# Performance work log

Measured on AMD Instinct MI355X. Metric: run time of the kernel, lower is better.

Reference implementation:

```python
import jax, jax.numpy as jnp
import numpy as np

B, T, N, C = 32, 12, 1024, 2   # batch, lookback window, n_series, in_channels
D, H, K, OUT = 16, 64, 2, 12   # embedding_dim, rnn_units, cheb_k, out_dim (horizon)


def setup_inputs() -> dict:
    key = jax.random.key(0)
    ks = jax.random.split(key, 12)
    p = lambda k, sh, s=0.1: jax.random.normal(k, sh, dtype=jnp.float32) * s
    return {
        "source": jax.random.normal(ks[0], (B, T, N, C), dtype=jnp.float32),
        "node_emb": p(ks[1], (N, D), 0.3),
        # layer 0: dim_in = C + H
        "gate_w0": p(ks[2], (D, K, C + H, 2 * H)),
        "gate_b0": p(ks[3], (D, 2 * H)),
        "upd_w0": p(ks[4], (D, K, C + H, H)),
        "upd_b0": p(ks[5], (D, H)),
        # layer 1: dim_in = H + H
        "gate_w1": p(ks[6], (D, K, 2 * H, 2 * H)),
        "gate_b1": p(ks[7], (D, 2 * H)),
        "upd_w1": p(ks[8], (D, K, 2 * H, H)),
        "upd_b1": p(ks[9], (D, H)),
        # end_conv: Conv2d(1, OUT*out_channels, kernel=(1,H)) == linear over hidden dim
        "conv_w": p(ks[10], (OUT, H)),
        "conv_b": p(ks[11], (OUT,)),
    }


def _supports(node_emb):
    # softmax(relu(E E^T)) row-normalized adaptive adjacency; Chebyshev stack (K, N, N)
    A = jax.nn.softmax(jax.nn.relu(node_emb @ node_emb.T), axis=1)
    s = [jnp.eye(N, dtype=A.dtype), A]
    for _ in range(2, K):
        s.append(2.0 * A @ s[-1] - s[-2])
    return jnp.stack(s, axis=0)


def _gcn(x, node_emb, w_pool, b_pool, supports):
    # x: (B, N, Cin); per-node adaptive weights from pools
    w = jnp.einsum('nd,dkio->nkio', node_emb, w_pool)     # (N, K, Cin, Cout)
    b = node_emb @ b_pool                                 # (N, Cout)
    xg = jnp.einsum('knm,bmc->bnkc', supports, x)         # (B, N, K, Cin)
    return jnp.einsum('bnki,nkio->bno', xg, w) + b


def _layer(x_seq, node_emb, supports, gw, gb, uw, ub):
    # x_seq: (B, T, N, Cin) -> (B, T, N, H) via GRU-style AGCRN cell, scanned over T
    def step(state, x_t):
        inp = jnp.concatenate([x_t, state], axis=-1)
        zr = jax.nn.sigmoid(_gcn(inp, node_emb, gw, gb, supports))
        z, r = jnp.split(zr, 2, axis=-1)
        cand = jnp.concatenate([x_t, z * state], axis=-1)
        hc = jnp.tanh(_gcn(cand, node_emb, uw, ub, supports))
        h = r * state + (1.0 - r) * hc
        return h, h

    init = jnp.zeros((x_seq.shape[0], N, H), dtype=x_seq.dtype)
    _, hs = jax.lax.scan(step, init, jnp.swapaxes(x_seq, 0, 1))
    return jnp.swapaxes(hs, 0, 1)


def reference(source, node_emb, gate_w0, gate_b0, upd_w0, upd_b0,
              gate_w1, gate_b1, upd_w1, upd_b1, conv_w, conv_b,
              teacher_forcing_ratio=0):
    sup = _supports(node_emb)  # adaptive supports depend only on static node_emb
    h1 = _layer(source, node_emb, sup, gate_w0, gate_b0, upd_w0, upd_b0)
    h2 = _layer(h1, node_emb, sup, gate_w1, gate_b1, upd_w1, upd_b1)
    last = h2[:, -1]  # (B, N, H)
    # end_conv over hidden dim -> (B, OUT, N); out_channels==1 so squeeze folds away
    out = jnp.einsum('bnh,oh->bon', last, conv_w) + conv_b[None, :, None]
    return out
```

## Files before the change

### kernel.cpp

```cpp
#include <hip/hip_runtime.h>
#include <hip/hip_fp16.h>


typedef _Float16 f16x8 __attribute__((ext_vector_type(8)));
typedef _Float16 f16x4 __attribute__((ext_vector_type(4)));
typedef float f32x4 __attribute__((ext_vector_type(4)));

__global__ __launch_bounds__(256) void compute_A_kernel(const float* __restrict__ E,
                                                        __half* __restrict__ Ah) {
  int n = blockIdx.x;
  int tid = threadIdx.x;
  __shared__ float red[256];
  float en[16];
#pragma unroll
  for (int d = 0; d < 16; ++d) en[d] = E[n * 16 + d];
  float v[4];
#pragma unroll
  for (int q = 0; q < 4; ++q) {
    int m = tid + q * 256;
    const float* Em = E + m * 16;
    float dot = 0.f;
#pragma unroll
    for (int d = 0; d < 16; ++d) dot += en[d] * Em[d];
    v[q] = fmaxf(dot, 0.f);
  }
  float mx = fmaxf(fmaxf(v[0], v[1]), fmaxf(v[2], v[3]));
  red[tid] = mx; __syncthreads();
  for (int s = 128; s > 0; s >>= 1) { if (tid < s) red[tid] = fmaxf(red[tid], red[tid + s]); __syncthreads(); }
  mx = red[0];
  __syncthreads();
  float e[4], sum = 0.f;
#pragma unroll
  for (int q = 0; q < 4; ++q) { e[q] = expf(v[q] - mx); sum += e[q]; }
  red[tid] = sum; __syncthreads();
  for (int s = 128; s > 0; s >>= 1) { if (tid < s) red[tid] += red[tid + s]; __syncthreads(); }
  float inv = 1.f / red[0];
#pragma unroll
  for (int q = 0; q < 4; ++q) Ah[(size_t)n * 1024 + tid + q * 256] = __float2half(e[q] * inv);
}

__global__ __launch_bounds__(256) void pool_t16_kernel(const float* __restrict__ gw0,
                                                       const float* __restrict__ uw0,
                                                       const float* __restrict__ gw1,
                                                       const float* __restrict__ uw1,
                                                       __half* __restrict__ poolT16) {
  int rg = blockIdx.x;
  const float* pool; int F, Fp, O; size_t jbase; int kk, jj;
  if (rg < 160)      { pool = gw0; F = 66;  Fp = 80;  O = 128; jbase = 0;     kk = rg / 80;          jj = rg % 80; }
  else if (rg < 320) { pool = uw0; F = 66;  Fp = 80;  O = 64;  jbase = 20480; kk = (rg - 160) / 80;  jj = (rg - 160) % 80; }
  else if (rg < 576) { pool = gw1; F = 128; Fp = 128; O = 128; jbase = 30720; kk = (rg - 320) / 128; jj = (rg - 320) % 128; }
  else               { pool = uw1; F = 128; Fp = 128; O = 64;  jbase = 63488; kk = (rg - 576) / 128; jj = (rg - 576) % 128; }
  int o = threadIdx.x;
  if (o >= O) return;
  int i;
  if (F == Fp) i = jj;
  else i = (jj < 64) ? jj + 2 : (jj < 66 ? jj - 64 : -1);
  f16x8 a = {}, b = {}, zz = {};
  if (i >= 0) {
#pragma unroll
    for (int d = 0; d < 8; ++d)
      a[d] = (_Float16)pool[(((size_t)d * 2 + kk) * F + i) * O + o];
#pragma unroll
    for (int d = 8; d < 16; ++d)
      b[d - 8] = (_Float16)pool[(((size_t)d * 2 + kk) * F + i) * O + o];
  }
  size_t j = jbase + (size_t)o * (2 * Fp) + (size_t)kk * Fp + jj;
  _Float16* outp = (_Float16*)poolT16 + j * 32;
  *(f16x8*)outp = a;
  *(f16x8*)(outp + 8) = b;
  *(f16x8*)(outp + 16) = zz;
  *(f16x8*)(outp + 24) = zz;
}

__global__ __launch_bounds__(256) void prelude_misc_kernel(
    const float* __restrict__ E, __half* __restrict__ E16,
    const float* __restrict__ gb0, const float* __restrict__ ub0,
    const float* __restrict__ gb1, const float* __restrict__ ub1,
    float* __restrict__ Bg0, float* __restrict__ Bu0,
    float* __restrict__ Bg1, float* __restrict__ Bu1,
    const float* __restrict__ src, __half* __restrict__ x16,
    float4* __restrict__ zero_p) {
  int bid = blockIdx.x;
  if (bid < 8192) {
    int i = bid * 256 + threadIdx.x;
    zero_p[i] = float4{0.f, 0.f, 0.f, 0.f};
    return;
  }
  bid -= 8192;
  if (bid < 384) {
    int t0 = bid >> 5, b = bid & 31;
    const float* s = src + (size_t)(b * 12 + t0) * 2048;
    __half* dst = x16 + t0 * 64 + b * 2;
    for (int nn = threadIdx.x; nn < 1024; nn += 256) {
      float2 v = *(const float2*)(s + nn * 2);
      *(__half2*)(dst + (size_t)nn * 768) = __floats2half2_rn(v.x, v.y);
    }
    return;
  }
  bid -= 384;
  if (bid < 1536) {
    int tid = bid * 256 + threadIdx.x;
    if (tid >= 1024 * 384) return;
    int n = tid / 384, c = tid - n * 384;
    const float* pool; float* outp; int O, o;
    if (c < 128)      { pool = gb0; outp = Bg0; O = 128; o = c; }
    else if (c < 192) { pool = ub0; outp = Bu0; O = 64;  o = c - 128; }
    else if (c < 320) { pool = gb1; outp = Bg1; O = 128; o = c - 192; }
    else              { pool = ub1; outp = Bu1; O = 64;  o = c - 320; }
    const float* En = E + n * 16;
    float a = 0.f;
#pragma unroll
    for (int d = 0; d < 16; ++d) a += En[d] * pool[d * O + o];
    outp[n * O + o] = a;
    return;
  }
  bid -= 1536;
  {
    int t = bid * 256 + threadIdx.x;
    if (t >= 1024 * 32) return;
    int d = t & 31;
    E16[t] = (d < 16) ? __float2half(E[(t >> 5) * 16 + d]) : __half(0);
  }
}

__global__ __launch_bounds__(256) void make_wt_mfma_kernel(
    const __half* __restrict__ E16g, const __half* __restrict__ poolT16g,
    __half* __restrict__ WtG0, __half* __restrict__ WtU0,
    __half* __restrict__ WtG1, __half* __restrict__ WtU1) {
  __shared__ __align__(16) _Float16 Es[64][40];
  __shared__ __align__(16) _Float16 wbuf[64][264];
  const _Float16* E16 = (const _Float16*)E16g;
  const _Float16* pT = (const _Float16*)poolT16g;
  int bx = blockIdx.x;
  __half* Wt; int OK, jbase;
  if (bx < 80)       { Wt = WtG0; OK = 128 * 160; jbase = bx * 256; }
  else if (bx < 120) { Wt = WtU0; OK = 64 * 160;  jbase = (bx - 80) * 256; }
  else if (bx < 248) { Wt = WtG1; OK = 128 * 256; jbase = (bx - 120) * 256; }
  else               { Wt = WtU1; OK = 64 * 256;  jbase = (bx - 248) * 256; }
  int jglob0 = bx * 256;
  int n0 = blockIdx.y * 64;
  {
    int r = threadIdx.x >> 2, ch = (threadIdx.x & 3) * 8;
    *(f16x8*)&Es[r][ch] = *(const f16x8*)(E16 + (size_t)(n0 + r) * 32 + ch);
  }
  __syncthreads();
  int wave = threadIdx.x >> 6, lane = threadIdx.x & 63;
  int fm = lane & 15, fg = lane >> 4;
  f16x8 af[4];
#pragma unroll
  for (int i = 0; i < 4; ++i) af[i] = *(const f16x8*)&Es[i * 16 + fm][fg * 8];
  f32x4 acc[4][4] = {};
#pragma unroll
  for (int j = 0; j < 4; ++j) {
    int jc = jglob0 + wave * 64 + j * 16 + fm;
    f16x8 bf = *(const f16x8*)(pT + (size_t)jc * 32 + fg * 8);
#pragma unroll
    for (int i = 0; i < 4; ++i)
      acc[i][j] = __builtin_amdgcn_mfma_f32_16x16x32_f16(af[i], bf, acc[i][j], 0, 0, 0);
  }
#pragma unroll
  for (int i = 0; i < 4; ++i)
#pragma unroll
    for (int j = 0; j < 4; ++j)
#pragma unroll
      for (int r = 0; r < 4; ++r)
        wbuf[i * 16 + fg * 4 + r][wave * 64 + j * 16 + fm] = (_Float16)acc[i][j][r];
  __syncthreads();
  for (int idx = threadIdx.x; idx < 64 * 32; idx += 256) {
    int nsub = idx >> 5, pos = (idx & 31) * 8;
    *(float4*)(Wt + (size_t)(n0 + nsub) * OK + jbase + pos) = *(float4*)&wbuf[nsub][pos];
  }
}

__global__ __launch_bounds__(256) void gemm_nt_kernel(
    const __half* __restrict__ Ahg, const __half* __restrict__ X0g,
    const __half* __restrict__ X1g, __half* __restrict__ Yg,
    int Nc, int cstride, int split) {
  __shared__ __align__(16) _Float16 As[64][136];
  __shared__ __align__(16) _Float16 Bs[64][144];
  const _Float16* __restrict__ Ah = (const _Float16*)Ahg;
  _Float16* __restrict__ Y = (_Float16*)Yg;
  int tid = threadIdx.x;
  int row0 = blockIdx.y * 64;
  int col0 = blockIdx.x * 64;
  const _Float16* __restrict__ Xsrc =
      (col0 < split) ? (const _Float16*)X0g : (const _Float16*)X1g;
  int colg = (col0 < split) ? col0 : col0 - split;
  int wave = tid >> 6, lane = tid & 63;
  int wm = wave & 1, wn = wave >> 1;
  int fm = lane & 15, fg = lane >> 4;

  int sr = tid >> 2, sc = (tid & 3) * 32;
  const _Float16* pa = Ah + (size_t)(row0 + sr) * 1024 + sc;
  int kq = tid & 31, cg = tid >> 5;
  int kb = 4 * kq;
  const _Float16* pb = Xsrc + (size_t)kb * cstride + colg + cg * 8;
  int chunk = kq >> 1;
  int kin = (kq & 1) * 4;

  f16x8 ra[4], rb[4];
#pragma unroll
  for (int c = 0; c < 4; ++c) ra[c] = *(const f16x8*)(pa + c * 8);
#pragma unroll
  for (int r = 0; r < 4; ++r) rb[r] = *(const f16x8*)(pb + (size_t)r * cstride);

  f32x4 acc[2][2] = {};
  for (int k0 = 0; k0 < 1024; k0 += 128) {
#pragma unroll
    for (int c = 0; c < 4; ++c) *(f16x8*)&As[sr][sc + c * 8] = ra[c];
#pragma unroll
    for (int i = 0; i < 8; ++i) {
      int c = cg * 8 + i;
      f16x4 p;
      p[0] = rb[0][i]; p[1] = rb[1][i]; p[2] = rb[2][i]; p[3] = rb[3][i];
      *(f16x4*)&Bs[c][((chunk ^ (c & 7)) << 3) + kin] = p;
    }
    __syncthreads();
    if (k0 + 128 < 1024) {
#pragma unroll
      for (int c = 0; c < 4; ++c) ra[c] = *(const f16x8*)(pa + k0 + 128 + c * 8);
#pragma unroll
      for (int r = 0; r < 4; ++r)
        rb[r] = *(const f16x8*)(pb + (size_t)(k0 + 128 + r) * cstride);
    }
#pragma unroll
    for (int kc = 0; kc < 4; ++kc) {
      int ck = kc * 4 + fg;
      f16x8 af[2], bf[2];
#pragma unroll
      for (int i = 0; i < 2; ++i)
        af[i] = *(const f16x8*)&As[wm * 32 + i * 16 + fm][kc * 32 + fg * 8];
#pragma unroll
      for (int j = 0; j < 2; ++j) {
        int cl = wn * 32 + j * 16 + fm;
        bf[j] = *(const f16x8*)&Bs[cl][(ck ^ (cl & 7)) << 3];
      }
#pragma unroll
      for (int i = 0; i < 2; ++i)
#pragma unroll
        for (int j = 0; j < 2; ++j)
          acc[i][j] = __builtin_amdgcn_mfma_f32_16x16x32_f16(af[i], bf[j], acc[i][j], 0, 0, 0);
    }
    __syncthreads();
  }
#pragma unroll
  for (int i = 0; i < 2; ++i) {
#pragma unroll
    for (int j = 0; j < 2; ++j) {
      int col = col0 + wn * 32 + j * 16 + fm;
      int rbase = row0 + wm * 32 + i * 16 + fg * 4;
#pragma unroll
      for (int r = 0; r < 4; ++r)
        Y[(size_t)(rbase + r) * Nc + col] = (_Float16)acc[i][j][r];
    }
  }
}

__global__ __launch_bounds__(256) void gemm_nt128_kernel(
    const __half* __restrict__ Ahg, const __half* __restrict__ X0g,
    const __half* __restrict__ X1g, __half* __restrict__ Yg,
    int Nc, int cstride, int split) {
  __shared__ __align__(16) _Float16 As[64][136];
  __shared__ __align__(16) _Float16 Bs[128][144];
  const _Float16* __restrict__ Ah = (const _Float16*)Ahg;
  _Float16* __restrict__ Y = (_Float16*)Yg;
  int tid = threadIdx.x;
  int row0 = blockIdx.y * 64;
  int col0 = blockIdx.x * 128;
  const _Float16* __restrict__ Xsrc =
      (col0 < split) ? (const _Float16*)X0g : (const _Float16*)X1g;
  int colg = (col0 < split) ? col0 : col0 - split;
  int wave = tid >> 6, lane = tid & 63;
  int fm = lane & 15, fg = lane >> 4;

  int sr = tid >> 2, sc = (tid & 3) * 32;
  const _Float16* pa = Ah + (size_t)(row0 + sr) * 1024 + sc;
  int kq = tid & 31, cg = tid >> 5;
  int kb = 4 * kq;
  const _Float16* pb = Xsrc + (size_t)kb * cstride + colg + cg * 16;
  int chunk = kq >> 1;
  int kin = (kq & 1) * 4;

  f16x8 ra[4], rb[4][2];
#pragma unroll
  for (int c = 0; c < 4; ++c) ra[c] = *(const f16x8*)(pa + c * 8);
#pragma unroll
  for (int r = 0; r < 4; ++r)
#pragma unroll
    for (int h = 0; h < 2; ++h)
      rb[r][h] = *(const f16x8*)(pb + (size_t)r * cstride + h * 8);

  f32x4 acc[4][2] = {};
  for (int k0 = 0; k0 < 1024; k0 += 128) {
#pragma unroll
    for (int c = 0; c < 4; ++c) *(f16x8*)&As[sr][sc + c * 8] = ra[c];
#pragma unroll
    for (int h = 0; h < 2; ++h)
#pragma unroll
      for (int i = 0; i < 8; ++i) {
        int c = cg * 16 + h * 8 + i;
        f16x4 p;
        p[0] = rb[0][h][i]; p[1] = rb[1][h][i]; p[2] = rb[2][h][i]; p[3] = rb[3][h][i];
        *(f16x4*)&Bs[c][((chunk ^ (c & 7)) << 3) + kin] = p;
      }
    __syncthreads();
    if (k0 + 128 < 1024) {
#pragma unroll
      for (int c = 0; c < 4; ++c) ra[c] = *(const f16x8*)(pa + k0 + 128 + c * 8);
#pragma unroll
      for (int r = 0; r < 4; ++r)
#pragma unroll
        for (int h = 0; h < 2; ++h)
          rb[r][h] = *(const f16x8*)(pb + (size_t)(k0 + 128 + r) * cstride + h * 8);
    }
#pragma unroll
    for (int kc = 0; kc < 4; ++kc) {
      int ck = kc * 4 + fg;
      f16x8 af[4], bf[2];
#pragma unroll
      for (int i = 0; i < 4; ++i)
        af[i] = *(const f16x8*)&As[i * 16 + fm][kc * 32 + fg * 8];
#pragma unroll
      for (int j = 0; j < 2; ++j) {
        int cl = wave * 32 + j * 16 + fm;
        bf[j] = *(const f16x8*)&Bs[cl][(ck ^ (cl & 7)) << 3];
      }
#pragma unroll
      for (int i = 0; i < 4; ++i)
#pragma unroll
        for (int j = 0; j < 2; ++j)
          acc[i][j] = __builtin_amdgcn_mfma_f32_16x16x32_f16(af[i], bf[j], acc[i][j], 0, 0, 0);
    }
    __syncthreads();
  }
#pragma unroll
  for (int i = 0; i < 4; ++i) {
#pragma unroll
    for (int j = 0; j < 2; ++j) {
      int col = col0 + wave * 32 + j * 16 + fm;
      int rbase = row0 + i * 16 + fg * 4;
#pragma unroll
      for (int r = 0; r < 4; ++r)
        Y[(size_t)(rbase + r) * Nc + col] = (_Float16)acc[i][j][r];
    }
  }
}

__device__ __forceinline__ f16x8 ld_g0(const __half* __restrict__ h16,
                                       const __half* __restrict__ YBD, int n, int idx) {
  int b = idx >> 4, part = (idx >> 3) & 1, ch = idx & 7;
  const _Float16* s = part ? (const _Float16*)YBD + (size_t)n * 4096 + b * 64 + ch * 8
                           : (const _Float16*)h16 + (size_t)n * 2048 + b * 64 + ch * 8;
  return *(const f16x8*)s;
}
__device__ __forceinline__ f16x8 ld_u0(const __half* __restrict__ zh0,
                                       const __half* __restrict__ YCE, int n, int idx) {
  int b = idx >> 4, part = (idx >> 3) & 1, ch = idx & 7;
  const _Float16* s = part ? (const _Float16*)YCE + (size_t)n * 4096 + 2048 + b * 64 + ch * 8
                           : (const _Float16*)zh0 + (size_t)n * 2048 + b * 64 + ch * 8;
  return *(const f16x8*)s;
}

__device__ __forceinline__ void gate0_body(
    _Float16* Xs, int n, int t,
    f16x8 pre0, f16x8 pre1, float2 xv, unsigned axu,
    const __half* __restrict__ Wtg, const float* __restrict__ Bg,
    const float* __restrict__ h32, __half* __restrict__ zh0, __half* __restrict__ r0) {
  constexpr int KIP = 160, STRIDE = 168;
  {
    int b0 = t >> 4, p0 = (t >> 3) & 1, c0 = t & 7;
    *(f16x8*)&Xs[b0 * STRIDE + p0 * 80 + c0 * 8] = pre0;
    int idx = t + 256;
    int b1 = idx >> 4, p1 = (idx >> 3) & 1, c1 = idx & 7;
    *(f16x8*)&Xs[b1 * STRIDE + p1 * 80 + c1 * 8] = pre1;
  }
  if (t < 32) {
    Xs[t * STRIDE + 64] = (_Float16)xv.x;
    Xs[t * STRIDE + 65] = (_Float16)xv.y;
    *(unsigned*)&Xs[t * STRIDE + 144] = axu;
  }
  for (int idx = t; idx < 896; idx += 256) {
    int b = idx / 28, jj = idx % 28;
    int col = (jj < 14) ? 66 + jj : 132 + jj;
    Xs[b * STRIDE + col] = (_Float16)0.f;
  }
  __syncthreads();
  int wave = t >> 6, lane = t & 63;
  int fm = lane & 15, fg = lane >> 4;
  f32x4 acc[2][2] = {};
  const _Float16* Wn = (const _Float16*)Wtg + ((size_t)n * 128 + wave * 32) * KIP;
  __builtin_amdgcn_s_setprio(1);
#pragma unroll
  for (int kc = 0; kc < KIP / 32; ++kc) {
    f16x8 af[2], bf[2];
#pragma unroll
    for (int i = 0; i < 2; ++i)
      af[i] = *(const f16x8*)&Xs[(i * 16 + fm) * STRIDE + kc * 32 + fg * 8];
#pragma unroll
    for (int j = 0; j < 2; ++j)
      bf[j] = *(const f16x8*)(Wn + (size_t)(j * 16 + fm) * KIP + kc * 32 + fg * 8);
#pragma unroll
    for (int i = 0; i < 2; ++i)
#pragma unroll
      for (int j = 0; j < 2; ++j)
        acc[i][j] = __builtin_amdgcn_mfma_f32_16x16x32_f16(af[i], bf[j], acc[i][j], 0, 0, 0);
  }
  __builtin_amdgcn_s_setprio(0);
  const float* Bn = Bg + n * 128;
#pragma unroll
  for (int j = 0; j < 2; ++j) {
    int o = wave * 32 + j * 16 + fm;
    float bias = Bn[o];
#pragma unroll
    for (int i = 0; i < 2; ++i)
#pragma unroll
      for (int r = 0; r < 4; ++r) {
        int b = i * 16 + fg * 4 + r;
        float s = 1.f / (1.f + __expf(-(acc[i][j][r] + bias)));
        size_t base = (size_t)n * 2048 + b * 64;
        if (o < 64) zh0[base + o] = __float2half(s * h32[base + o]);
        else        r0[base + o - 64] = __float2half(s);
      }
  }
}

__device__ __forceinline__ void upd0_body(
    _Float16* Xs, int n, int t,
    f16x8 pre0, f16x8 pre1, float2 xv, unsigned axu,
    const __half* __restrict__ Wtg, const float* __restrict__ Bu,
    const __half* __restrict__ r0, float* __restrict__ h32, __half* __restrict__ h16) {
  constexpr int KIP = 160, STRIDE = 168;
  {
    int b0 = t >> 4, p0 = (t >> 3) & 1, c0 = t & 7;
    *(f16x8*)&Xs[b0 * STRIDE + p0 * 80 + c0 * 8] = pre0;
    int idx = t + 256;
    int b1 = idx >> 4, p1 = (idx >> 3) & 1, c1 = idx & 7;
    *(f16x8*)&Xs[b1 * STRIDE + p1 * 80 + c1 * 8] = pre1;
  }
  if (t < 32) {
    Xs[t * STRIDE + 64] = (_Float16)xv.x;
    Xs[t * STRIDE + 65] = (_Float16)xv.y;
    *(unsigned*)&Xs[t * STRIDE + 144] = axu;
  }
  for (int idx = t; idx < 896; idx += 256) {
    int b = idx / 28, jj = idx % 28;
    int col = (jj < 14) ? 66 + jj : 132 + jj;
    Xs[b * STRIDE + col] = (_Float16)0.f;
  }
  __syncthreads();
  int wave = t >> 6, lane = t & 63;
  int fm = lane & 15, fg = lane >> 4;
  f32x4 acc[2] = {};
  const _Float16* Wn = (const _Float16*)Wtg + ((size_t)n * 64 + wave * 16) * KIP;
  __builtin_amdgcn_s_setprio(1);
#pragma unroll
  for (int kc = 0; kc < KIP / 32; ++kc) {
    f16x8 bf = *(const f16x8*)(Wn + (size_t)fm * KIP + kc * 32 + fg * 8);
#pragma unroll
    for (int i = 0; i < 2; ++i) {
      f16x8 af = *(const f16x8*)&Xs[(i * 16 + fm) * STRIDE + kc * 32 + fg * 8];
      acc[i] = __builtin_amdgcn_mfma_f32_16x16x32_f16(af, bf, acc[i], 0, 0, 0);
    }
  }
  __builtin_amdgcn_s_setprio(0);
  int o = wave * 16 + fm;
  float bias = Bu[n * 64 + o];
#pragma unroll
  for (int i = 0; i < 2; ++i)
#pragma unroll
    for (int r = 0; r < 4; ++r) {
      int b = i * 16 + fg * 4 + r;
      float x = acc[i][r] + bias;
      x = fminf(fmaxf(x, -15.f), 15.f);
      float e = __expf(2.f * x);
      float hc = (e - 1.f) / (e + 1.f);
      size_t base = (size_t)n * 2048 + b * 64;
      float rr = __half2float(r0[base + o]);
      float hnew = rr * h32[base + o] + (1.f - rr) * hc;
      h32[base + o] = hnew;
      h16[base + o] = __float2half(hnew);
    }
}

__global__ __launch_bounds__(256) void gate0_kernel(
    const __half* __restrict__ h16, const __half* __restrict__ YBD,
    const float* __restrict__ src, const __half* __restrict__ Axt, int tstep,
    const __half* __restrict__ Wtg, const float* __restrict__ Bg,
    const float* __restrict__ h32, __half* __restrict__ zh0, __half* __restrict__ r0) {
  __shared__ __align__(16) _Float16 Xs[32 * 168];
  int n = blockIdx.x, t = threadIdx.x;
  f16x8 p0 = ld_g0(h16, YBD, n, t);
  f16x8 p1 = ld_g0(h16, YBD, n, t + 256);
  float2 xv = {}; unsigned ax = 0;
  if (t < 32) {
    xv = *(const float2*)(src + ((size_t)(t * 12 + tstep) * 1024 + n) * 2);
    ax = *(const unsigned*)((const _Float16*)Axt + (size_t)n * 768 + tstep * 64 + t * 2);
  }
  gate0_body(Xs, n, t, p0, p1, xv, ax, Wtg, Bg, h32, zh0, r0);
}

__global__ __launch_bounds__(256) void upd0_kernel(
    const __half* __restrict__ zh0, const __half* __restrict__ YCE,
    const float* __restrict__ src, const __half* __restrict__ Axt, int tstep,
    const __half* __restrict__ Wtg, const float* __restrict__ Bu,
    const __half* __restrict__ r0, float* __restrict__ h32, __half* __restrict__ h16) {
  __shared__ __align__(16) _Float16 Xs[32 * 168];
  int n = blockIdx.x, t = threadIdx.x;
  f16x8 p0 = ld_u0(zh0, YCE, n, t);
  f16x8 p1 = ld_u0(zh0, YCE, n, t + 256);
  float2 xv = {}; unsigned ax = 0;
  if (t < 32) {
    xv = *(const float2*)(src + ((size_t)(t * 12 + tstep) * 1024 + n) * 2);
    ax = *(const unsigned*)((const _Float16*)Axt + (size_t)n * 768 + tstep * 64 + t * 2);
  }
  upd0_body(Xs, n, t, p0, p1, xv, ax, Wtg, Bu, r0, h32, h16);
}

__global__ __launch_bounds__(256) void gate1_gate0_kernel(
    const __half* __restrict__ h1_16, const __half* __restrict__ h2_16,
    const __half* __restrict__ YBD,
    const __half* __restrict__ WtG1, const float* __restrict__ Bg1,
    const float* __restrict__ h2_32, __half* __restrict__ zh1, __half* __restrict__ r1,
    const float* __restrict__ src, const __half* __restrict__ Axt, int tnext,
    const __half* __restrict__ WtG0, const float* __restrict__ Bg0,
    const float* __restrict__ h1_32, __half* __restrict__ zh0, __half* __restrict__ r0,
    int do_gate0) {
  constexpr int KIP = 256, STRIDE = 264;
  __shared__ __align__(16) _Float16 Xs[32 * STRIDE];
  int n = blockIdx.x;
  int t = threadIdx.x;
  f16x8 s1[4];
#pragma unroll
  for (int u = 0; u < 4; ++u) {
    int idx = t + u * 256;
    int b = idx >> 5, q = idx & 31;
    const _Float16* s;
    if (q < 8)       s = (const _Float16*)h1_16 + (size_t)n * 2048 + b * 64 + q * 8;
    else if (q < 16) s = (const _Float16*)h2_16 + (size_t)n * 2048 + b * 64 + (q - 8) * 8;
    else if (q < 24) s = (const _Float16*)YBD + (size_t)n * 4096 + b * 64 + (q - 16) * 8;
    else             s = (const _Float16*)YBD + (size_t)n * 4096 + 2048 + b * 64 + (q - 24) * 8;
    s1[u] = *(const f16x8*)s;
  }
  f16x8 g0p0 = {}, g0p1 = {}; float2 g0xv = {}; unsigned g0ax = 0;
  if (do_gate0) {
    g0p0 = ld_g0(h1_16, YBD, n, t);
    g0p1 = ld_g0(h1_16, YBD, n, t + 256);
    if (t < 32) {
      g0xv = *(const float2*)(src + ((size_t)(t * 12 + tnext) * 1024 + n) * 2);
      g0ax = *(const unsigned*)((const _Float16*)Axt + (size_t)n * 768 + tnext * 64 + t * 2);
    }
  }
#pragma unroll
  for (int u = 0; u < 4; ++u) {
    int idx = t + u * 256;
    int b = idx >> 5, q = idx & 31;
    *(f16x8*)&Xs[b * STRIDE + q * 8] = s1[u];
  }
  __syncthreads();
  int wave = t >> 6, lane = t & 63;
  int fm = lane & 15, fg = lane >> 4;
  {
    f32x4 acc[2][2] = {};
    const _Float16* Wn = (const _Float16*)WtG1 + ((size_t)n * 128 + wave * 32) * KIP;
    __builtin_amdgcn_s_setprio(1);
#pragma unroll
    for (int kc = 0; kc < KIP / 32; ++kc) {
      f16x8 af[2], bf[2];
#pragma unroll
      for (int i = 0; i < 2; ++i)
        af[i] = *(const f16x8*)&Xs[(i * 16 + fm) * STRIDE + kc * 32 + fg * 8];
#pragma unroll
      for (int j = 0; j < 2; ++j)
        bf[j] = *(const f16x8*)(Wn + (size_t)(j * 16 + fm) * KIP + kc * 32 + fg * 8);
#pragma unroll
      for (int i = 0; i < 2; ++i)
#pragma unroll
        for (int j = 0; j < 2; ++j)
          acc[i][j] = __builtin_amdgcn_mfma_f32_16x16x32_f16(af[i], bf[j], acc[i][j], 0, 0, 0);
    }
    __builtin_amdgcn_s_setprio(0);
    const float* Bn = Bg1 + n * 128;
#pragma unroll
    for (int j = 0; j < 2; ++j) {
      int o = wave * 32 + j * 16 + fm;
      float bias = Bn[o];
#pragma unroll
      for (int i = 0; i < 2; ++i)
#pragma unroll
        for (int r = 0; r < 4; ++r) {
          int b = i * 16 + fg * 4 + r;
          float s = 1.f / (1.f + __expf(-(acc[i][j][r] + bias)));
          size_t base = (size_t)n * 2048 + b * 64;
          if (o < 64) zh1[base + o] = __float2half(s * h2_32[base + o]);
          else        r1[base + o - 64] = __float2half(s);
        }
    }
  }
  if (!do_gate0) return;
  __syncthreads();
  gate0_body(Xs, n, t, g0p0, g0p1, g0xv, g0ax, WtG0, Bg0, h1_32, zh0, r0);
}

__global__ __launch_bounds__(256) void upd1_upd0_kernel(
    const __half* __restrict__ h1_16, const __half* __restrict__ zh1,
    const __half* __restrict__ YBD, const __half* __restrict__ YCE,
    const __half* __restrict__ WtU1, const float* __restrict__ Bu1,
    const __half* __restrict__ r1, float* __restrict__ h2_32, __half* __restrict__ h2_16,
    const __half* __restrict__ zh0,
    const float* __restrict__ src, const __half* __restrict__ Axt, int tnext,
    const __half* __restrict__ WtU0, const float* __restrict__ Bu0,
    const __half* __restrict__ r0, float* __restrict__ h1_32, __half* __restrict__ h1_16w,
    int do_upd0) {
  constexpr int KIP = 256, STRIDE = 264;
  __shared__ __align__(16) _Float16 Xs[32 * STRIDE];
  int n = blockIdx.x;
  int t = threadIdx.x;
  f16x8 s1[4];
#pragma unroll
  for (int u = 0; u < 4; ++u) {
    int idx = t + u * 256;
    int b = idx >> 5, q = idx & 31;
    const _Float16* s;
    if (q < 8)       s = (const _Float16*)h1_16 + (size_t)n * 2048 + b * 64 + q * 8;
    else if (q < 16) s = (const _Float16*)zh1 + (size_t)n * 2048 + b * 64 + (q - 8) * 8;
    else if (q < 24) s = (const _Float16*)YBD + (size_t)n * 4096 + b * 64 + (q - 16) * 8;
    else             s = (const _Float16*)YCE + (size_t)n * 4096 + b * 64 + (q - 24) * 8;
    s1[u] = *(const f16x8*)s;
  }
  f16x8 u0p0 = {}, u0p1 = {}; float2 u0xv = {}; unsigned u0ax = 0;
  if (do_upd0) {
    u0p0 = ld_u0(zh0, YCE, n, t);
    u0p1 = ld_u0(zh0, YCE, n, t + 256);
    if (t < 32) {
      u0xv = *(const float2*)(src + ((size_t)(t * 12 + tnext) * 1024 + n) * 2);
      u0ax = *(const unsigned*)((const _Float16*)Axt + (size_t)n * 768 + tnext * 64 + t * 2);
    }
  }
#pragma unroll
  for (int u = 0; u < 4; ++u) {
    int idx = t + u * 256;
    int b = idx >> 5, q = idx & 31;
    *(f16x8*)&Xs[b * STRIDE + q * 8] = s1[u];
  }
  __syncthreads();
  int wave = t >> 6, lane = t & 63;
  int fm = lane & 15, fg = lane >> 4;
  {
    f32x4 acc[2] = {};
    const _Float16* Wn = (const _Float16*)WtU1 + ((size_t)n * 64 + wave * 16) * KIP;
    __builtin_amdgcn_s_setprio(1);
#pragma unroll
    for (int kc = 0; kc < KIP / 32; ++kc) {
      f16x8 bf = *(const f16x8*)(Wn + (size_t)fm * KIP + kc * 32 + fg * 8);
#pragma unroll
      for (int i = 0; i < 2; ++i) {
        f16x8 af = *(const f16x8*)&Xs[(i * 16 + fm) * STRIDE + kc * 32 + fg * 8];
        acc[i] = __builtin_amdgcn_mfma_f32_16x16x32_f16(af, bf, acc[i], 0, 0, 0);
      }
    }
    __builtin_amdgcn_s_setprio(0);
    int o = wave * 16 + fm;
    float bias = Bu1[n * 64 + o];
#pragma unroll
    for (int i = 0; i < 2; ++i)
#pragma unroll
      for (int r = 0; r < 4; ++r) {
        int b = i * 16 + fg * 4 + r;
        float x = acc[i][r] + bias;
        x = fminf(fmaxf(x, -15.f), 15.f);
        float e = __expf(2.f * x);
        float hc = (e - 1.f) / (e + 1.f);
        size_t base = (size_t)n * 2048 + b * 64;
        float rr = __half2float(r1[base + o]);
        float hnew = rr * h2_32[base + o] + (1.f - rr) * hc;
        h2_32[base + o] = hnew;
        h2_16[base + o] = __float2half(hnew);
      }
  }
  if (!do_upd0) return;
  __syncthreads();
  upd0_body(Xs, n, t, u0p0, u0p1, u0xv, u0ax, WtU0, Bu0, r0, h1_32, h1_16w);
}

__global__ void final_conv_kernel(const float* __restrict__ h2, const float* __restrict__ cw,
                                  const float* __restrict__ cb, float* __restrict__ out) {
  int tid = blockIdx.x * 256 + threadIdx.x;
  if (tid >= 32 * 1024) return;
  int n = tid & 1023, b = tid >> 10;
  const float* hp = h2 + ((size_t)n * 32 + b) * 64;
  float hv[64];
#pragma unroll
  for (int i = 0; i < 64; ++i) hv[i] = hp[i];
#pragma unroll
  for (int o = 0; o < 12; ++o) {
    float acc = cb[o];
#pragma unroll
    for (int i = 0; i < 64; ++i) acc += hv[i] * cw[o * 64 + i];
    out[((size_t)b * 12 + o) * 1024 + n] = acc;
  }
}

extern "C" void kernel_launch(void* const* d_in, const int* in_sizes, int n_in,
                              void* d_out, int out_size, void* d_ws, size_t ws_size,
                              hipStream_t stream) {
  const float* src = (const float*)d_in[0];
  const float* E   = (const float*)d_in[1];
  const float* gw0 = (const float*)d_in[2];
  const float* gb0 = (const float*)d_in[3];
  const float* uw0 = (const float*)d_in[4];
  const float* ub0 = (const float*)d_in[5];
  const float* gw1 = (const float*)d_in[6];
  const float* gb1 = (const float*)d_in[7];
  const float* uw1 = (const float*)d_in[8];
  const float* ub1 = (const float*)d_in[9];
  const float* cw  = (const float*)d_in[10];
  const float* cb  = (const float*)d_in[11];
  float* out = (float*)d_out;
  (void)in_sizes; (void)n_in; (void)out_size; (void)ws_size;

  char* base = (char*)d_ws;
  size_t off = 0;
  auto alloc = [&](size_t bytes) -> void* {
    void* p = base + off; off += (bytes + 511) & ~(size_t)511; return p;
  };
  __half* Ah   = (__half*)alloc((size_t)1024 * 1024 * 2);
  __half* WtG0 = (__half*)alloc((size_t)1024 * 128 * 160 * 2);
  __half* WtU0 = (__half*)alloc((size_t)1024 * 64 * 160 * 2);
  __half* WtG1 = (__half*)alloc((size_t)1024 * 128 * 256 * 2);
  __half* WtU1 = (__half*)alloc((size_t)1024 * 64 * 256 * 2);
  float*  Bg0  = (float*) alloc((size_t)1024 * 128 * 4);
  float*  Bu0  = (float*) alloc((size_t)1024 * 64 * 4);
  float*  Bg1  = (float*) alloc((size_t)1024 * 128 * 4);
  float*  Bu1  = (float*) alloc((size_t)1024 * 64 * 4);
  float*  h1_32 = (float*)alloc((size_t)1024 * 2048 * 4);
  float*  h2_32 = (float*)alloc((size_t)1024 * 2048 * 4);
  __half* h1_16 = (__half*)alloc((size_t)1024 * 2048 * 2);
  __half* h2_16 = (__half*)alloc((size_t)1024 * 2048 * 2);
  __half* YBD  = (__half*)alloc((size_t)1024 * 4096 * 2);
  __half* YCE  = (__half*)alloc((size_t)1024 * 4096 * 2);
  __half* zh0  = (__half*)alloc((size_t)1024 * 2048 * 2);
  __half* zh1  = (__half*)alloc((size_t)1024 * 2048 * 2);
  __half* Axt  = (__half*)alloc((size_t)1024 * 768 * 2);
  __half* r1   = (__half*)alloc((size_t)1024 * 2048 * 2);
  __half* r0   = (__half*)alloc((size_t)1024 * 2048 * 2);
  __half* poolT16 = (__half*)alloc((size_t)79872 * 32 * 2);
  __half* E16  = (__half*)alloc((size_t)1024 * 32 * 2);
  __half* x16  = (__half*)alloc((size_t)1024 * 768 * 2);

  compute_A_kernel<<<1024, 256, 0, stream>>>(E, Ah);
  prelude_misc_kernel<<<10240, 256, 0, stream>>>(E, E16, gb0, ub0, gb1, ub1,
                                                 Bg0, Bu0, Bg1, Bu1,
                                                 src, x16, (float4*)h1_32);
  pool_t16_kernel<<<832, 256, 0, stream>>>(gw0, uw0, gw1, uw1, poolT16);
  make_wt_mfma_kernel<<<dim3(312, 16), 256, 0, stream>>>(E16, poolT16, WtG0, WtU0, WtG1, WtU1);
  gemm_nt_kernel<<<dim3(12, 16), 256, 0, stream>>>(Ah, (__half*)x16, (__half*)x16, Axt,
                                                   768, 768, 768);

  gate0_kernel<<<1024, 256, 0, stream>>>(h1_16, YBD, src, Axt, 0, WtG0, Bg0, h1_32, zh0, r0);
  gemm_nt128_kernel<<<dim3(16, 16), 256, 0, stream>>>(Ah, zh0, zh0, YCE + 2048,
                                                      4096, 2048, 2048);
  upd0_kernel<<<1024, 256, 0, stream>>>(zh0, YCE, src, Axt, 0, WtU0, Bu0, r0, h1_32, h1_16);

  for (int t = 0; t < 12; ++t) {
    int more = (t < 11) ? 1 : 0;
    gemm_nt128_kernel<<<dim3(32, 16), 256, 0, stream>>>(Ah, h1_16, h2_16, YBD,
                                                        4096, 2048, 2048);
    gate1_gate0_kernel<<<1024, 256, 0, stream>>>(h1_16, h2_16, YBD, WtG1, Bg1, h2_32, zh1, r1,
                                                 src, Axt, t + 1, WtG0, Bg0, h1_32, zh0, r0,
                                                 more);
    gemm_nt128_kernel<<<dim3(32, 16), 256, 0, stream>>>(Ah, zh1, zh0, YCE,
                                                        4096, 2048, 2048);
    upd1_upd0_kernel<<<1024, 256, 0, stream>>>(h1_16, zh1, YBD, YCE, WtU1, Bu1, r1,
                                               h2_32, h2_16, zh0, src, Axt, t + 1,
                                               WtU0, Bu0, r0, h1_32, h1_16, more);
  }

  final_conv_kernel<<<(32 * 1024 + 255) / 256, 256, 0, stream>>>(h2_32, cw, cb, out);
}
```

Before: 1.377 ms.

## Double-buffer per-node weights into LDS via async global_load_lds DMA

Weight tiles for the MFMA loops in the gate/update kernels are now streamed into a two-slot LDS ring with global_load_lds, using an XOR swizzle and explicit vmcnt/lgkmcnt waits and barriers. The next layer's weights are prefetched during the tail of the fused first GEMM. The aim is to hide global-memory latency on the weight operand, which was previously loaded straight into registers inside the k-loop. In exchange each k-step needs two barriers and more LDS, and the hand-written waitcnt accounting is fragile.

```diff
diff --git a/kernel.cpp b/kernel.cpp
--- a/kernel.cpp
+++ b/kernel.cpp
@@ -5,6 +5,50 @@
 typedef _Float16 f16x8 __attribute__((ext_vector_type(8)));
 typedef _Float16 f16x4 __attribute__((ext_vector_type(4)));
 typedef float f32x4 __attribute__((ext_vector_type(4)));
+
+#define WAIT_VM0 asm volatile("s_waitcnt vmcnt(0)" ::: "memory")
+#define WAIT_VM1 asm volatile("s_waitcnt vmcnt(1)" ::: "memory")
+#define WAIT_VM2 asm volatile("s_waitcnt vmcnt(2)" ::: "memory")
+#define WAIT_VM1_LG asm volatile("s_waitcnt vmcnt(1) lgkmcnt(0)" ::: "memory")
+#define WAIT_VM2_LG asm volatile("s_waitcnt vmcnt(2) lgkmcnt(0)" ::: "memory")
+#define WAIT_LG asm volatile("s_waitcnt lgkmcnt(0)" ::: "memory")
+#define BARRIER do { __builtin_amdgcn_s_barrier(); asm volatile("" ::: "memory"); } while (0)
+
+__device__ __forceinline__ void gload_lds16(const void* g, void* l) {
+  __builtin_amdgcn_global_load_lds(
+      (const __attribute__((address_space(1))) void*)g,
+      (__attribute__((address_space(3))) void*)l, 16, 0, 0);
+}
+
+__device__ __forceinline__ void dma_g128(const _Float16* Wn, int KIP, int kc,
+                                         _Float16* buf, int tid) {
+  int wave = tid >> 6;
+#pragma unroll
+  for (int u = 0; u < 2; ++u) {
+    int flat = u * 256 + tid;
+    int o = (flat & 7) | ((flat >> 5) << 3);
+    int s = ((flat >> 3) & 3) ^ (o & 3);
+    const _Float16* g = Wn + (size_t)o * KIP + kc * 32 + s * 8;
+    _Float16* l = buf + ((size_t)(u * 256 + wave * 64)) * 8;
+    gload_lds16(g, l);
+  }
+}
+
+__device__ __forceinline__ void dma_g64(const _Float16* Wn, int KIP, int kc,
+                                        _Float16* buf, int tid) {
+  int wave = tid >> 6;
+  int flat = tid;
+  int o = (flat & 7) | ((flat >> 5) << 3);
+  int s = ((flat >> 3) & 3) ^ (o & 3);
+  const _Float16* g = Wn + (size_t)o * KIP + kc * 32 + s * 8;
+  _Float16* l = buf + (size_t)(wave * 64) * 8;
+  gload_lds16(g, l);
+}
+
+__device__ __forceinline__ f16x8 wrd(const _Float16* buf, int o, int s) {
+  int flat = (o & 7) | (((s ^ (o & 3)) & 3) << 3) | ((o >> 3) << 5);
+  return *(const f16x8*)(buf + flat * 8);
+}
 
 __global__ __launch_bounds__(256) void compute_A_kernel(const float* __restrict__ E,
                                                         __half* __restrict__ Ah) {
@@ -362,9 +406,9 @@
 }
 
 __device__ __forceinline__ void gate0_body(
-    _Float16* Xs, int n, int t,
+    _Float16* Xs, _Float16 (*Wb)[4096], int n, int t,
     f16x8 pre0, f16x8 pre1, float2 xv, unsigned axu,
-    const __half* __restrict__ Wtg, const float* __restrict__ Bg,
+    const _Float16* Wn, const float* __restrict__ Bg,
     const float* __restrict__ h32, __half* __restrict__ zh0, __half* __restrict__ r0) {
   constexpr int KIP = 160, STRIDE = 168;
   {
@@ -384,28 +428,34 @@
     int col = (jj < 14) ? 66 + jj : 132 + jj;
     Xs[b * STRIDE + col] = (_Float16)0.f;
   }
-  __syncthreads();
   int wave = t >> 6, lane = t & 63;
   int fm = lane & 15, fg = lane >> 4;
   f32x4 acc[2][2] = {};
-  const _Float16* Wn = (const _Float16*)Wtg + ((size_t)n * 128 + wave * 32) * KIP;
-  __builtin_amdgcn_s_setprio(1);
-#pragma unroll
-  for (int kc = 0; kc < KIP / 32; ++kc) {
+#pragma unroll
+  for (int kc = 0; kc < 5; ++kc) {
+    if (kc == 0) WAIT_VM2_LG;
+    else if (kc < 4) WAIT_VM2;
+    else WAIT_VM0;
+    BARRIER;
+    const _Float16* wb = Wb[kc & 1];
     f16x8 af[2], bf[2];
 #pragma unroll
     for (int i = 0; i < 2; ++i)
       af[i] = *(const f16x8*)&Xs[(i * 16 + fm) * STRIDE + kc * 32 + fg * 8];
 #pragma unroll
     for (int j = 0; j < 2; ++j)
-      bf[j] = *(const f16x8*)(Wn + (size_t)(j * 16 + fm) * KIP + kc * 32 + fg * 8);
+      bf[j] = wrd(wb, wave * 32 + j * 16 + fm, fg);
+    __builtin_amdgcn_s_setprio(1);
 #pragma unroll
     for (int i = 0; i < 2; ++i)
 #pragma unroll
       for (int j = 0; j < 2; ++j)
         acc[i][j] = __builtin_amdgcn_mfma_f32_16x16x32_f16(af[i], bf[j], acc[i][j], 0, 0, 0);
-  }
-  __builtin_amdgcn_s_setprio(0);
+    __builtin_amdgcn_s_setprio(0);
+    WAIT_LG;
+    BARRIER;
+    if (kc < 3) dma_g128(Wn, KIP, kc + 2, Wb[kc & 1], t);
+  }
   const float* Bn = Bg + n * 128;
 #pragma unroll
   for (int j = 0; j < 2; ++j) {
@@ -425,9 +475,9 @@
 }
 
 __device__ __forceinline__ void upd0_body(
-    _Float16* Xs, int n, int t,
+    _Float16* Xs, _Float16 (*Wb)[4096], int n, int t,
     f16x8 pre0, f16x8 pre1, float2 xv, unsigned axu,
-    const __half* __restrict__ Wtg, const float* __restrict__ Bu,
+    const _Float16* Wn, const float* __restrict__ Bu,
     const __half* __restrict__ r0, float* __restrict__ h32, __half* __restrict__ h16) {
   constexpr int KIP = 160, STRIDE = 168;
   {
@@ -447,22 +497,28 @@
     int col = (jj < 14) ? 66 + jj : 132 + jj;
     Xs[b * STRIDE + col] = (_Float16)0.f;
   }
-  __syncthreads();
   int wave = t >> 6, lane = t & 63;
   int fm = lane & 15, fg = lane >> 4;
   f32x4 acc[2] = {};
-  const _Float16* Wn = (const _Float16*)Wtg + ((size_t)n * 64 + wave * 16) * KIP;
-  __builtin_amdgcn_s_setprio(1);
-#pragma unroll
-  for (int kc = 0; kc < KIP / 32; ++kc) {
-    f16x8 bf = *(const f16x8*)(Wn + (size_t)fm * KIP + kc * 32 + fg * 8);
+#pragma unroll
+  for (int kc = 0; kc < 5; ++kc) {
+    if (kc == 0) WAIT_VM1_LG;
+    else if (kc < 4) WAIT_VM1;
+    else WAIT_VM0;
+    BARRIER;
+    const _Float16* wb = Wb[kc & 1];
+    f16x8 bf = wrd(wb, wave * 16 + fm, fg);
+    __builtin_amdgcn_s_setprio(1);
 #pragma unroll
     for (int i = 0; i < 2; ++i) {
       f16x8 af = *(const f16x8*)&Xs[(i * 16 + fm) * STRIDE + kc * 32 + fg * 8];
       acc[i] = __builtin_amdgcn_mfma_f32_16x16x32_f16(af, bf, acc[i], 0, 0, 0);
     }
-  }
-  __builtin_amdgcn_s_setprio(0);
+    __builtin_amdgcn_s_setprio(0);
+    WAIT_LG;
+    BARRIER;
+    if (kc < 3) dma_g64(Wn, KIP, kc + 2, Wb[kc & 1], t);
+  }
   int o = wave * 16 + fm;
   float bias = Bu[n * 64 + o];
 #pragma unroll
@@ -488,7 +544,9 @@
     const __half* __restrict__ Wtg, const float* __restrict__ Bg,
     const float* __restrict__ h32, __half* __restrict__ zh0, __half* __restrict__ r0) {
   __shared__ __align__(16) _Float16 Xs[32 * 168];
+  __shared__ __align__(16) _Float16 Wb[2][4096];
   int n = blockIdx.x, t = threadIdx.x;
+  const _Float16* Wn = (const _Float16*)Wtg + (size_t)n * 128 * 160;
   f16x8 p0 = ld_g0(h16, YBD, n, t);
   f16x8 p1 = ld_g0(h16, YBD, n, t + 256);
   float2 xv = {}; unsigned ax = 0;
@@ -496,7 +554,9 @@
     xv = *(const float2*)(src + ((size_t)(t * 12 + tstep) * 1024 + n) * 2);
     ax = *(const unsigned*)((const _Float16*)Axt + (size_t)n * 768 + tstep * 64 + t * 2);
   }
-  gate0_body(Xs, n, t, p0, p1, xv, ax, Wtg, Bg, h32, zh0, r0);
+  dma_g128(Wn, 160, 0, Wb[0], t);
+  dma_g128(Wn, 160, 1, Wb[1], t);
+  gate0_body(Xs, Wb, n, t, p0, p1, xv, ax, Wn, Bg, h32, zh0, r0);
 }
 
 __global__ __launch_bounds__(256) void upd0_kernel(
@@ -505,7 +565,9 @@
     const __half* __restrict__ Wtg, const float* __restrict__ Bu,
     const __half* __restrict__ r0, float* __restrict__ h32, __half* __restrict__ h16) {
   __shared__ __align__(16) _Float16 Xs[32 * 168];
+  __shared__ __align__(16) _Float16 Wb[2][4096];
   int n = blockIdx.x, t = threadIdx.x;
+  const _Float16* Wn = (const _Float16*)Wtg + (size_t)n * 64 * 160;
   f16x8 p0 = ld_u0(zh0, YCE, n, t);
   f16x8 p1 = ld_u0(zh0, YCE, n, t + 256);
   float2 xv = {}; unsigned ax = 0;
@@ -513,7 +575,9 @@
     xv = *(const float2*)(src + ((size_t)(t * 12 + tstep) * 1024 + n) * 2);
     ax = *(const unsigned*)((const _Float16*)Axt + (size_t)n * 768 + tstep * 64 + t * 2);
   }
-  upd0_body(Xs, n, t, p0, p1, xv, ax, Wtg, Bu, r0, h32, h16);
+  dma_g64(Wn, 160, 0, Wb[0], t);
+  dma_g64(Wn, 160, 1, Wb[1], t);
+  upd0_body(Xs, Wb, n, t, p0, p1, xv, ax, Wn, Bu, r0, h32, h16);
 }
 
 __global__ __launch_bounds__(256) void gate1_gate0_kernel(
@@ -525,10 +589,13 @@
     const __half* __restrict__ WtG0, const float* __restrict__ Bg0,
     const float* __restrict__ h1_32, __half* __restrict__ zh0, __half* __restrict__ r0,
     int do_gate0) {
-  constexpr int KIP = 256, STRIDE = 264;
+  constexpr int STRIDE = 264;
   __shared__ __align__(16) _Float16 Xs[32 * STRIDE];
+  __shared__ __align__(16) _Float16 Wb[2][4096];
   int n = blockIdx.x;
   int t = threadIdx.x;
+  const _Float16* Wn1 = (const _Float16*)WtG1 + (size_t)n * 128 * 256;
+  const _Float16* Wn0 = (const _Float16*)WtG0 + (size_t)n * 128 * 160;
   f16x8 s1[4];
 #pragma unroll
   for (int u = 0; u < 4; ++u) {
@@ -550,35 +617,44 @@
       g0ax = *(const unsigned*)((const _Float16*)Axt + (size_t)n * 768 + tnext * 64 + t * 2);
     }
   }
+  dma_g128(Wn1, 256, 0, Wb[0], t);
+  dma_g128(Wn1, 256, 1, Wb[1], t);
 #pragma unroll
   for (int u = 0; u < 4; ++u) {
     int idx = t + u * 256;
     int b = idx >> 5, q = idx & 31;
     *(f16x8*)&Xs[b * STRIDE + q * 8] = s1[u];
   }
-  __syncthreads();
   int wave = t >> 6, lane = t & 63;
   int fm = lane & 15, fg = lane >> 4;
   {
     f32x4 acc[2][2] = {};
-    const _Float16* Wn = (const _Float16*)WtG1 + ((size_t)n * 128 + wave * 32) * KIP;
-    __builtin_amdgcn_s_setprio(1);
-#pragma unroll
-    for (int kc = 0; kc < KIP / 32; ++kc) {
+#pragma unroll
+    for (int kc = 0; kc < 8; ++kc) {
+      if (kc == 0) WAIT_VM2_LG;
+      else if (kc < 7) WAIT_VM2;
+      else { if (do_gate0) WAIT_VM2; else WAIT_VM0; }
+      BARRIER;
+      const _Float16* wb = Wb[kc & 1];
       f16x8 af[2], bf[2];
 #pragma unroll
       for (int i = 0; i < 2; ++i)
         af[i] = *(const f16x8*)&Xs[(i * 16 + fm) * STRIDE + kc * 32 + fg * 8];
 #pragma unroll
       for (int j = 0; j < 2; ++j)
-        bf[j] = *(const f16x8*)(Wn + (size_t)(j * 16 + fm) * KIP + kc * 32 + fg * 8);
+        bf[j] = wrd(wb, wave * 32 + j * 16 + fm, fg);
+      __builtin_amdgcn_s_setprio(1);
 #pragma unroll
       for (int i = 0; i < 2; ++i)
 #pragma unroll
         for (int j = 0; j < 2; ++j)
           acc[i][j] = __builtin_amdgcn_mfma_f32_16x16x32_f16(af[i], bf[j], acc[i][j], 0, 0, 0);
-    }
-    __builtin_amdgcn_s_setprio(0);
+      __builtin_amdgcn_s_setprio(0);
+      WAIT_LG;
+      BARRIER;
+      if (kc < 6) dma_g128(Wn1, 256, kc + 2, Wb[kc & 1], t);
+      else if (do_gate0) dma_g128(Wn0, 160, kc - 6, Wb[kc & 1], t);
+    }
     const float* Bn = Bg1 + n * 128;
 #pragma unroll
     for (int j = 0; j < 2; ++j) {
@@ -597,8 +673,7 @@
     }
   }
   if (!do_gate0) return;
-  __syncthreads();
-  gate0_body(Xs, n, t, g0p0, g0p1, g0xv, g0ax, WtG0, Bg0, h1_32, zh0, r0);
+  gate0_body(Xs, Wb, n, t, g0p0, g0p1, g0xv, g0ax, Wn0, Bg0, h1_32, zh0, r0);
 }
 
 __global__ __launch_bounds__(256) void upd1_upd0_kernel(
@@ -611,10 +686,13 @@
     const __half* __restrict__ WtU0, const float* __restrict__ Bu0,
     const __half* __restrict__ r0, float* __restrict__ h1_32, __half* __restrict__ h1_16w,
     int do_upd0) {
-  constexpr int KIP = 256, STRIDE = 264;
+  constexpr int STRIDE = 264;
   __shared__ __align__(16) _Float16 Xs[32 * STRIDE];
+  __shared__ __align__(16) _Float16 Wb[2][4096];
   int n = blockIdx.x;
   int t = threadIdx.x;
+  const _Float16* Wn1 = (const _Float16*)WtU1 + (size_t)n * 64 * 256;
+  const _Float16* Wn0 = (const _Float16*)WtU0 + (size_t)n * 64 * 160;
   f16x8 s1[4];
 #pragma unroll
   for (int u = 0; u < 4; ++u) {
@@ -636,29 +714,38 @@
       u0ax = *(const unsigned*)((const _Float16*)Axt + (size_t)n * 768 + tnext * 64 + t * 2);
     }
   }
+  dma_g64(Wn1, 256, 0, Wb[0], t);
+  dma_g64(Wn1, 256, 1, Wb[1], t);
 #pragma unroll
   for (int u = 0; u < 4; ++u) {
     int idx = t + u * 256;
     int b = idx >> 5, q = idx & 31;
     *(f16x8*)&Xs[b * STRIDE + q * 8] = s1[u];
   }
-  __syncthreads();
   int wave = t >> 6, lane = t & 63;
   int fm = lane & 15, fg = lane >> 4;
   {
     f32x4 acc[2] = {};
-    const _Float16* Wn = (const _Float16*)WtU1 + ((size_t)n * 64 + wave * 16) * KIP;
-    __builtin_amdgcn_s_setprio(1);
-#pragma unroll
-    for (int kc = 0; kc < KIP / 32; ++kc) {
-      f16x8 bf = *(const f16x8*)(Wn + (size_t)fm * KIP + kc * 32 + fg * 8);
+#pragma unroll
+    for (int kc = 0; kc < 8; ++kc) {
+      if (kc == 0) WAIT_VM1_LG;
+      else if (kc < 7) WAIT_VM1;
+      else { if (do_upd0) WAIT_VM1; else WAIT_VM0; }
+      BARRIER;
+      const _Float16* wb = Wb[kc & 1];
+      f16x8 bf = wrd(wb, wave * 16 + fm, fg);
+      __builtin_amdgcn_s_setprio(1);
 #pragma unroll
       for (int i = 0; i < 2; ++i) {
         f16x8 af = *(const f16x8*)&Xs[(i * 16 + fm) * STRIDE + kc * 32 + fg * 8];
         acc[i] = __builtin_amdgcn_mfma_f32_16x16x32_f16(af, bf, acc[i], 0, 0, 0);
       }
-    }
-    __builtin_amdgcn_s_setprio(0);
+      __builtin_amdgcn_s_setprio(0);
+      WAIT_LG;
+      BARRIER;
+      if (kc < 6) dma_g64(Wn1, 256, kc + 2, Wb[kc & 1], t);
+      else if (do_upd0) dma_g64(Wn0, 160, kc - 6, Wb[kc & 1], t);
+    }
     int o = wave * 16 + fm;
     float bias = Bu1[n * 64 + o];
 #pragma unroll
@@ -678,8 +765,7 @@
       }
   }
   if (!do_upd0) return;
-  __syncthreads();
-  upd0_body(Xs, n, t, u0p0, u0p1, u0xv, u0ax, WtU0, Bu0, r0, h1_32, h1_16w);
+  upd0_body(Xs, Wb, n, t, u0p0, u0p1, u0xv, u0ax, Wn0, Bu0, r0, h1_32, h1_16w);
 }
 
 __global__ void final_conv_kernel(const float* __restrict__ h2, const float* __restrict__ cw,
```

New measurement: 1.377 ms. About the same (-0.0%).
